# Optimization experiments

Hardware: AMD Instinct MI355X
Metric: run time of the kernel (lower is better)

Reference implementation:

```python
import jax, jax.numpy as jnp
import numpy as np

B, L, E = 2, 2048, 1024
H = 16
DH = E // H  # head dim for qk and v (dim_qk=dim_v=embed_dim)
HID = 4 * E  # fcn_dim_factor * dim_v
SCALE = DH ** 0.5


def setup_inputs() -> dict:
    key = jax.random.key(0)
    ks = jax.random.split(key, 12)
    s = lambda fan_in: 1.0 / np.sqrt(fan_in)
    return {
        "x": jax.random.uniform(ks[0], (B, L), jnp.float32),
        "z": jax.random.normal(ks[1], (B, L, E), jnp.float32),
        "Wq": jax.random.normal(ks[2], (E, E), jnp.float32) * s(E),
        "bq": jnp.zeros((E,), jnp.float32),
        "Wk": jax.random.normal(ks[3], (E, E), jnp.float32) * s(E),
        "bk": jnp.zeros((E,), jnp.float32),
        "Wv": jax.random.normal(ks[4], (E, E), jnp.float32) * s(E),
        "bv": jnp.zeros((E,), jnp.float32),
        "W1": jax.random.normal(ks[5], (E, HID), jnp.float32) * s(E),
        "b1": jnp.zeros((HID,), jnp.float32),
        "W2": jax.random.normal(ks[6], (HID, 1), jnp.float32) * s(HID),
        "b2": jnp.zeros((1,), jnp.float32),
    }


def reference(x, z, Wq, bq, Wk, bk, Wv, bv, W1, b1, W2, b2):
    # Projections -> (B, H, L, DH)
    def heads(t):
        return t.reshape(B, L, H, DH).transpose(0, 2, 1, 3)

    Q = heads(z @ Wq + bq)
    K = heads(z @ Wk + bk)
    V = heads(z @ Wv + bv)

    # Scores (B, H, L, L)
    S = jnp.einsum("bhid,bhjd->bhij", Q, K) / SCALE

    # Weighted softmax along query axis (dim=-2), weighted by population x
    w = x[:, None, :, None]  # (B, 1, L, 1), broadcasts over queries i
    m = jnp.max(S, axis=-2, keepdims=True)
    e = w * jnp.exp(S - m)
    A = e / jnp.sum(e, axis=-2, keepdims=True)

    # V scaled by population weight, then AV
    V_scaled = w * V
    O = jnp.einsum("bhij,bhjd->bhid", A, V_scaled)  # (B, H, L, DH)
    O = O.transpose(0, 2, 1, 3).reshape(B, L, H * DH)

    # FFN: Linear -> GELU (exact) -> Linear(->1) -> squeeze
    y = jax.nn.gelu(O @ W1 + b1, approximate=False)
    y = (y @ W2 + b2).squeeze(-1)  # (B, L)
    return y
```

## Files before the change

kernel.cpp:

```cpp
#include <hip/hip_runtime.h>
#include <hip/hip_bf16.h>
#include <math.h>

#define B_    2
#define L_    2048
#define E_    1024
#define H_    16
#define DH_   64
#define HID_  4096
#define NROW_ (B_*L_)
#define BH_   (B_*H_)

#define QSCL  0.18033688011112042f

typedef __attribute__((ext_vector_type(8)))  short    short8v;
typedef _Float16 half8v __attribute__((ext_vector_type(8)));
typedef __attribute__((ext_vector_type(16))) float    f32x16;

#define MFMA32(A, Bv, C) __builtin_amdgcn_mfma_f32_32x32x16_bf16((A), (Bv), (C), 0, 0, 0)
#define MFMAH(A, Bv, C)  __builtin_amdgcn_mfma_f32_32x32x16_f16((A), (Bv), (C), 0, 0, 0)

__device__ __forceinline__ unsigned short f2bf(float f) {
    union { float f; unsigned u; } v; v.f = f;
    return (unsigned short)((v.u + 0x8000u) >> 16);
}
__device__ __forceinline__ unsigned pack2_bf16(float lo, float hi) {
    union { float f; unsigned u; } a, b; a.f = lo; b.f = hi;
    return __builtin_amdgcn_perm(b.u + 0x8000u, a.u + 0x8000u, 0x07060302u);
}
__device__ __forceinline__ float bf2f(unsigned short u) {
    union { unsigned u; float f; } v; v.u = ((unsigned)u) << 16;
    return v.f;
}

__device__ __forceinline__ void gl_lds16(const void* g, void* l) {
    __builtin_amdgcn_global_load_lds(
        (const __attribute__((address_space(1))) unsigned int*)g,
        (__attribute__((address_space(3))) unsigned int*)l, 16, 0, 0);
}

__device__ __forceinline__ float erf_fast(float v) {
    float a = fabsf(v);
    float t = __builtin_amdgcn_rcpf(1.0f + 0.3275911f * a);
    float p = t * (0.254829592f + t * (-0.284496736f + t * (1.421413741f +
              t * (-1.453152027f + t * 1.061405429f))));
    float r = 1.0f - p * __expf(-a * a);
    return copysignf(r, v);
}

__global__ __launch_bounds__(256) void zh_prep(
    const float* __restrict__ z, _Float16* __restrict__ zh)
{
    const size_t i = ((size_t)blockIdx.x * 256 + threadIdx.x) * 8;
    float4 a = *(const float4*)&z[i];
    float4 b = *(const float4*)&z[i + 4];
    union { _Float16 h[8]; half8v v; } o;
    o.h[0] = (_Float16)a.x; o.h[1] = (_Float16)a.y;
    o.h[2] = (_Float16)a.z; o.h[3] = (_Float16)a.w;
    o.h[4] = (_Float16)b.x; o.h[5] = (_Float16)b.y;
    o.h[6] = (_Float16)b.z; o.h[7] = (_Float16)b.w;
    *(half8v*)&zh[i] = o.v;
}

__global__ __launch_bounds__(256) void wprep3(
    const float* __restrict__ Wq, const float* __restrict__ Wk,
    const float* __restrict__ Wv,
    _Float16* __restrict__ Tq, _Float16* __restrict__ Tk,
    _Float16* __restrict__ Tv)
{
    const float* src = (blockIdx.z == 0) ? Wq : (blockIdx.z == 1) ? Wk : Wv;
    _Float16*    dst = (blockIdx.z == 0) ? Tq : (blockIdx.z == 1) ? Tk : Tv;
    __shared__ float tile[64][65];
    const int t  = threadIdx.x;
    const int r0 = blockIdx.y * 64, c0 = blockIdx.x * 64;
    #pragma unroll
    for (int u = 0; u < 4; ++u) {
        int f = t + 256 * u, row = f >> 4, c4 = (f & 15) << 2;
        *(float4*)&tile[row][c4] = *(const float4*)&src[(size_t)(r0 + row) * E_ + c0 + c4];
    }
    __syncthreads();
    #pragma unroll
    for (int u = 0; u < 4; ++u) {
        int f = t + 256 * u, c = f >> 4, r4 = (f & 15) << 2;
        union { _Float16 h[4]; uint2 u2; } pk;
        pk.h[0] = (_Float16)tile[r4 + 0][c];
        pk.h[1] = (_Float16)tile[r4 + 1][c];
        pk.h[2] = (_Float16)tile[r4 + 2][c];
        pk.h[3] = (_Float16)tile[r4 + 3][c];
        *(uint2*)&dst[(size_t)(c0 + c) * E_ + r0 + r4] = pk.u2;
    }
}

__global__ __launch_bounds__(256) void w1prep(
    const float* __restrict__ W1, _Float16* __restrict__ W1t)
{
    __shared__ float tile[64][65];
    const int t  = threadIdx.x;
    const int r0 = blockIdx.y * 64, c0 = blockIdx.x * 64;
    #pragma unroll
    for (int u = 0; u < 4; ++u) {
        int f = t + 256 * u, row = f >> 4, c4 = (f & 15) << 2;
        *(float4*)&tile[row][c4] = *(const float4*)&W1[(size_t)(r0 + row) * HID_ + c0 + c4];
    }
    __syncthreads();
    #pragma unroll
    for (int u = 0; u < 4; ++u) {
        int f = t + 256 * u, c = f >> 4, r4 = (f & 15) << 2;
        union { _Float16 h[4]; uint2 u2; } pk;
        pk.h[0] = (_Float16)tile[r4 + 0][c];
        pk.h[1] = (_Float16)tile[r4 + 1][c];
        pk.h[2] = (_Float16)tile[r4 + 2][c];
        pk.h[3] = (_Float16)tile[r4 + 3][c];
        *(uint2*)&W1t[(size_t)(c0 + c) * E_ + r0 + r4] = pk.u2;
    }
}

__global__ __launch_bounds__(256) void qkv_mfma(
    const _Float16* __restrict__ zh,
    const _Float16* __restrict__ Tq, const _Float16* __restrict__ Tk,
    const _Float16* __restrict__ Tv,
    const float* __restrict__ bq, const float* __restrict__ bk,
    const float* __restrict__ bv,
    unsigned short* __restrict__ Qo, unsigned short* __restrict__ Ko,
    unsigned short* __restrict__ Vo)
{
    const int which = blockIdx.z;
    const _Float16* Wt = (which == 0) ? Tq : (which == 1) ? Tk : Tv;
    const float*  bias = (which == 0) ? bq : (which == 1) ? bk : bv;
    unsigned short* out = (which == 0) ? Qo : (which == 1) ? Ko : Vo;
    const float   osc  = (which == 0) ? QSCL : 1.0f;

    __shared__ _Float16 Ah[128 * 64];
    __shared__ _Float16 Bs[128 * 64];

    const int t    = threadIdx.x;
    const int lane = t & 63;
    const int w    = t >> 6;
    const int l31  = lane & 31;
    const int hq   = lane >> 5;
    const int wm   = w >> 1, wn = w & 1;
    const int m0   = blockIdx.x * 128;
    const int n0   = blockIdx.y * 128;

    const int srow0 = (lane >> 3);
    const int ssl   = lane & 7;

    f32x16 acc[2][2] = {};

    for (int kc = 0; kc < 16; ++kc) {
        __syncthreads();
        #pragma unroll
        for (int u = 0; u < 4; ++u) {
            int ch  = w * 4 + u;
            int row = ch * 8 + srow0;
            gl_lds16(&zh[(size_t)(m0 + row) * E_ + kc * 64 + ((ssl ^ (row & 7)) << 3)], &Ah[ch * 512]);
            gl_lds16(&Wt[(size_t)(n0 + row) * E_ + kc * 64 + ((ssl ^ (row & 7)) << 3)], &Bs[ch * 512]);
        }
        __syncthreads();

        #pragma unroll
        for (int ks = 0; ks < 4; ++ks) {
            half8v fb[2];
            #pragma unroll
            for (int nb = 0; nb < 2; ++nb) {
                int br = wn * 64 + nb * 32 + l31;
                fb[nb] = *(const half8v*)&Bs[br * 64 + (((ks * 2 + hq) ^ (br & 7)) << 3)];
            }
            #pragma unroll
            for (int mb = 0; mb < 2; ++mb) {
                int ar = wm * 64 + mb * 32 + l31;
                half8v fa = *(const half8v*)&Ah[ar * 64 + (((ks * 2 + hq) ^ (ar & 7)) << 3)];
                acc[mb][0] = MFMAH(fa, fb[0], acc[mb][0]);
                acc[mb][1] = MFMAH(fa, fb[1], acc[mb][1]);
            }
        }
    }

    #pragma unroll
    for (int nb = 0; nb < 2; ++nb) {
        int n  = n0 + wn * 64 + nb * 32 + l31;
        int h  = n >> 6, dh = n & 63;
        float bb = bias[n];
        #pragma unroll
        for (int mb = 0; mb < 2; ++mb) {
            #pragma unroll
            for (int r = 0; r < 16; ++r) {
                int m  = m0 + wm * 64 + mb * 32 + (r & 3) + 8 * (r >> 2) + 4 * hq;
                int b  = m >> 11, i = m & (L_ - 1);
                out[((size_t)(b * H_ + h) * L_ + i) * DH_ + dh] = f2bf((acc[mb][nb][r] + bb) * osc);
            }
        }
    }
}

__global__ __launch_bounds__(256) void col_stats_mfma(
    const unsigned short* __restrict__ Qb, const unsigned short* __restrict__ Kb,
    const float* __restrict__ x, float* __restrict__ Do)
{
    __shared__ unsigned short Qlds[2][128 * 64];
    __shared__ float xlds[L_];

    const int t    = threadIdx.x;
    const int lane = t & 63;
    const int wv   = t >> 6;
    const int l31  = lane & 31;
    const int hq   = lane >> 5;
    const int bh   = blockIdx.y;
    const int b    = bh >> 4;
    const int j0   = blockIdx.x * 128 + wv * 32;

    const int srow0 = (lane >> 3);
    const int ssl   = lane & 7;

    #pragma unroll
    for (int u = 0; u < 2; ++u) {
        int f = t + 256 * u;
        *(float4*)&xlds[f * 4] = *(const float4*)&x[(size_t)b * L_ + f * 4];
    }

    short8v kf[4];
    {
        const unsigned short* kp = Kb + ((size_t)bh * L_ + j0 + l31) * DH_ + hq * 8;
        #pragma unroll
        for (int c = 0; c < 4; ++c) kf[c] = *(const short8v*)(kp + c * 16);
    }

    float d[16];
    #pragma unroll
    for (int r = 0; r < 16; ++r) d[r] = 0.f;

#define CS_STAGE(bb, ich)                                                           \
    {                                                                               \
        _Pragma("unroll")                                                           \
        for (int u = 0; u < 4; ++u) {                                               \
            int ch  = wv * 4 + u;                                                   \
            int row = ch * 8 + srow0;                                               \
            gl_lds16(&Qb[((size_t)bh * L_ + (ich) * 128 + row) * DH_ + ((ssl ^ (row & 7)) << 3)], \
                     &Qlds[bb][ch * 512]);                                          \
        }                                                                           \
    }

    CS_STAGE(0, 0);
    __syncthreads();
    int cur = 0;

    for (int ich = 0; ich < L_ / 128; ++ich) {
        if (ich < L_ / 128 - 1) CS_STAGE(cur ^ 1, ich + 1);

        #pragma unroll
        for (int cc = 0; cc < 4; ++cc) {
            f32x16 acc = {};
            __builtin_amdgcn_s_setprio(1);
            #pragma unroll
            for (int c = 0; c < 4; ++c) {
                int qr = cc * 32 + l31;
                short8v qv = *(const short8v*)&Qlds[cur][qr * 64 + (((c * 2 + hq) ^ (qr & 7)) << 3)];
                acc = MFMA32(kf[c], qv, acc);
            }
            __builtin_amdgcn_s_setprio(0);
            float xi = xlds[ich * 128 + cc * 32 + l31];
            #pragma unroll
            for (int r = 0; r < 16; ++r)
                d[r] += xi * __builtin_amdgcn_exp2f(acc[r]);
        }
        __syncthreads();
        cur ^= 1;
    }

    #pragma unroll
    for (int r = 0; r < 16; ++r) {
        #pragma unroll
        for (int off = 16; off > 0; off >>= 1)
            d[r] += __shfl_xor(d[r], off);
    }
    if (l31 == 0) {
        #pragma unroll
        for (int r = 0; r < 16; ++r)
            Do[(size_t)bh * L_ + j0 + 4 * hq + (r & 3) + 8 * (r >> 2)] = d[r];
    }
#undef CS_STAGE
}

__global__ __launch_bounds__(256) void vt_prep(
    const unsigned short* __restrict__ Vb, const float* __restrict__ x,
    const float* __restrict__ Do, unsigned short* __restrict__ Vt)
{
    const int bh = blockIdx.y;
    const int b  = bh >> 4;
    const int j  = blockIdx.x * 256 + threadIdx.x;
    const float s = x[(size_t)b * L_ + j] / Do[(size_t)bh * L_ + j];
    const unsigned short* vp = Vb + ((size_t)bh * L_ + j) * DH_;
    #pragma unroll
    for (int c = 0; c < 16; ++c) {
        ushort4 v = *(const ushort4*)&vp[c * 4];
        Vt[((size_t)bh * DH_ + c * 4 + 0) * L_ + j] = f2bf(bf2f(v.x) * s);
        Vt[((size_t)bh * DH_ + c * 4 + 1) * L_ + j] = f2bf(bf2f(v.y) * s);
        Vt[((size_t)bh * DH_ + c * 4 + 2) * L_ + j] = f2bf(bf2f(v.z) * s);
        Vt[((size_t)bh * DH_ + c * 4 + 3) * L_ + j] = f2bf(bf2f(v.w) * s);
    }
}

__global__ __launch_bounds__(256) void attn_out_mfma(
    const unsigned short* __restrict__ Qb, const unsigned short* __restrict__ Kb,
    const unsigned short* __restrict__ Vt, const float* __restrict__ x,
    _Float16* __restrict__ Of)
{
    __shared__ unsigned short Klds[2][64 * 64];
    __shared__ unsigned short Vlds[2][64 * 64];

    const int t    = threadIdx.x;
    const int lane = t & 63;
    const int wv   = t >> 6;
    const int l31  = lane & 31;
    const int hq   = lane >> 5;
    const int bh   = blockIdx.y;
    const int b    = bh >> 4, hh = bh & 15;
    const int iw   = blockIdx.x * 128 + wv * 32;

    const int srow0 = (lane >> 3);
    const int ssl   = lane & 7;

    short8v qf[4];
    {
        const unsigned short* qp = Qb + ((size_t)bh * L_ + iw + l31) * DH_ + hq * 8;
        #pragma unroll
        for (int c = 0; c < 4; ++c) qf[c] = *(const short8v*)(qp + c * 16);
    }

    f32x16 accO0 = {}, accO1 = {};

#define AO_STAGE(bb, jt)                                                            \
    {                                                                               \
        _Pragma("unroll")                                                           \
        for (int u = 0; u < 2; ++u) {                                               \
            int ch  = wv * 2 + u;                                                   \
            int row = ch * 8 + srow0;                                               \
            gl_lds16(&Kb[((size_t)bh * L_ + (jt) * 64 + row) * DH_ + ((ssl ^ (row & 7)) << 3)], \
                     &Klds[bb][ch * 512]);                                          \
            gl_lds16(&Vt[((size_t)bh * DH_ + row) * L_ + (jt) * 64 + ((ssl ^ (row & 7)) << 3)], \
                     &Vlds[bb][ch * 512]);                                          \
        }                                                                           \
    }

    AO_STAGE(0, 0);
    __syncthreads();
    int cur = 0;

    for (int jt = 0; jt < L_ / 64; ++jt) {
        if (jt < L_ / 64 - 1) AO_STAGE(cur ^ 1, jt + 1);

        uint4 pa[4];
        #pragma unroll
        for (int js = 0; js < 2; ++js) {
            f32x16 as = {};
            __builtin_amdgcn_s_setprio(1);
            #pragma unroll
            for (int c = 0; c < 4; ++c) {
                int krow = js * 32 + l31;
                short8v kfr = *(const short8v*)&Klds[cur][krow * 64 + (((c * 2 + hq) ^ (krow & 7)) << 3)];
                as = MFMA32(kfr, qf[c], as);
            }
            __builtin_amdgcn_s_setprio(0);
            float p[16];
            #pragma unroll
            for (int r = 0; r < 16; ++r) p[r] = __builtin_amdgcn_exp2f(as[r]);

            unsigned P0 = pack2_bf16(p[0], p[1]);
            unsigned P1 = pack2_bf16(p[2], p[3]);
            unsigned Q0 = pack2_bf16(p[4], p[5]);
            unsigned Q1 = pack2_bf16(p[6], p[7]);
            asm("v_permlane32_swap_b32 %0, %1" : "+v"(P0), "+v"(Q0));
            asm("v_permlane32_swap_b32 %0, %1" : "+v"(P1), "+v"(Q1));
            pa[js * 2 + 0] = make_uint4(P0, P1, Q0, Q1);

            unsigned R0 = pack2_bf16(p[8],  p[9]);
            unsigned R1 = pack2_bf16(p[10], p[11]);
            unsigned S0 = pack2_bf16(p[12], p[13]);
            unsigned S1 = pack2_bf16(p[14], p[15]);
            asm("v_permlane32_swap_b32 %0, %1" : "+v"(R0), "+v"(S0));
            asm("v_permlane32_swap_b32 %0, %1" : "+v"(R1), "+v"(S1));
            pa[js * 2 + 1] = make_uint4(R0, R1, S0, S1);
        }

        __builtin_amdgcn_s_setprio(1);
        #pragma unroll
        for (int c = 0; c < 4; ++c) {
            union { uint4 u; short8v s; } paf; paf.u = pa[c];
            int r0 = l31, r1 = 32 + l31;
            short8v vf0 = *(const short8v*)&Vlds[cur][r0 * 64 + (((c * 2 + hq) ^ (r0 & 7)) << 3)];
            short8v vf1 = *(const short8v*)&Vlds[cur][r1 * 64 + (((c * 2 + hq) ^ (r1 & 7)) << 3)];
            accO0 = MFMA32(paf.s, vf0, accO0);
            accO1 = MFMA32(paf.s, vf1, accO1);
        }
        __builtin_amdgcn_s_setprio(0);
        __syncthreads();
        cur ^= 1;
    }

    #pragma unroll
    for (int q = 0; q < 4; ++q) {
        float4 xq = *(const float4*)&x[(size_t)b * L_ + iw + 4 * hq + 8 * q];
        const float xs[4] = { xq.x, xq.y, xq.z, xq.w };
        #pragma unroll
        for (int k = 0; k < 4; ++k) {
            int r    = q * 4 + k;
            int irow = iw + 4 * hq + 8 * q + k;
            size_t base = ((size_t)b * L_ + irow) * E_ + hh * DH_;
            Of[base + l31]      = (_Float16)(accO0[r] * xs[k]);
            Of[base + 32 + l31] = (_Float16)(accO1[r] * xs[k]);
        }
    }
#undef AO_STAGE
}

__global__ __launch_bounds__(256) void y_init(float* __restrict__ y, const float* __restrict__ b2)
{
    y[blockIdx.x * 256 + threadIdx.x] = b2[0];
}

__global__ __launch_bounds__(256) void mlp_mfma(
    const _Float16* __restrict__ Of, const _Float16* __restrict__ W1t,
    const float* __restrict__ b1, const float* __restrict__ W2,
    float* __restrict__ y)
{
    __shared__ _Float16 Oh[128 * 64];
    __shared__ _Float16 Wh[128 * 64];

    const int t    = threadIdx.x;
    const int lane = t & 63;
    const int w    = t >> 6;
    const int l31  = lane & 31;
    const int hq   = lane >> 5;
    const int wm   = w >> 1, wn = w & 1;
    const int m0   = blockIdx.x * 128;
    const int n0   = blockIdx.y * 128;

    const int srow0 = (lane >> 3);
    const int ssl   = lane & 7;

    f32x16 acc[2][2] = {};

    for (int kc = 0; kc < 16; ++kc) {
        __syncthreads();
        #pragma unroll
        for (int u = 0; u < 4; ++u) {
            int ch  = w * 4 + u;
            int row = ch * 8 + srow0;
            gl_lds16(&Of[(size_t)(m0 + row) * E_ + kc * 64 + ((ssl ^ (row & 7)) << 3)], &Oh[ch * 512]);
            gl_lds16(&W1t[(size_t)(n0 + row) * E_ + kc * 64 + ((ssl ^ (row & 7)) << 3)], &Wh[ch * 512]);
        }
        __syncthreads();

        #pragma unroll
        for (int ks = 0; ks < 4; ++ks) {
            half8v fb[2];
            #pragma unroll
            for (int nb = 0; nb < 2; ++nb) {
                int br = wn * 64 + nb * 32 + l31;
                fb[nb] = *(const half8v*)&Wh[br * 64 + (((ks * 2 + hq) ^ (br & 7)) << 3)];
            }
            #pragma unroll
            for (int mb = 0; mb < 2; ++mb) {
                int ar = wm * 64 + mb * 32 + l31;
                half8v fa = *(const half8v*)&Oh[ar * 64 + (((ks * 2 + hq) ^ (ar & 7)) << 3)];
                acc[mb][0] = MFMAH(fa, fb[0], acc[mb][0]);
                acc[mb][1] = MFMAH(fa, fb[1], acc[mb][1]);
            }
        }
    }

    const int hid0 = n0 + wn * 64 + l31;
    const float bb0 = b1[hid0],      w20 = W2[hid0];
    const float bb1 = b1[hid0 + 32], w21 = W2[hid0 + 32];
    #pragma unroll
    for (int mb = 0; mb < 2; ++mb) {
        #pragma unroll
        for (int r = 0; r < 16; ++r) {
            float h0 = acc[mb][0][r] + bb0;
            float h1 = acc[mb][1][r] + bb1;
            float s  = 0.5f * h0 * (1.0f + erf_fast(h0 * 0.70710678f)) * w20
                     + 0.5f * h1 * (1.0f + erf_fast(h1 * 0.70710678f)) * w21;
            #pragma unroll
            for (int off = 16; off > 0; off >>= 1) s += __shfl_xor(s, off);
            if (l31 == 0) {
                int m = m0 + wm * 64 + mb * 32 + (r & 3) + 8 * (r >> 2) + 4 * hq;
                atomicAdd(&y[m], s);
            }
        }
    }
}

extern "C" void kernel_launch(void* const* d_in, const int* in_sizes, int n_in,
                              void* d_out, int out_size, void* d_ws, size_t ws_size,
                              hipStream_t stream)
{
    const float* x  = (const float*)d_in[0];
    const float* z  = (const float*)d_in[1];
    const float* Wq = (const float*)d_in[2];
    const float* bq = (const float*)d_in[3];
    const float* Wk = (const float*)d_in[4];
    const float* bk = (const float*)d_in[5];
    const float* Wv = (const float*)d_in[6];
    const float* bv = (const float*)d_in[7];
    const float* W1 = (const float*)d_in[8];
    const float* b1 = (const float*)d_in[9];
    const float* W2 = (const float*)d_in[10];
    const float* b2 = (const float*)d_in[11];
    float* y = (float*)d_out;

    const size_t NQ = (size_t)BH_ * L_ * DH_;
    unsigned short* p = (unsigned short*)d_ws;
    unsigned short* Qb  = p;  p += NQ;
    unsigned short* Kb  = p;  p += NQ;
    unsigned short* Vb  = p;  p += NQ;
    unsigned short* Vt  = p;  p += NQ;
    _Float16* zh  = (_Float16*)p;  p += (size_t)NROW_ * E_;
    _Float16* Tq  = (_Float16*)p;  p += (size_t)E_ * E_;
    _Float16* Tk  = (_Float16*)p;  p += (size_t)E_ * E_;
    _Float16* Tv  = (_Float16*)p;  p += (size_t)E_ * E_;
    _Float16* W1t = (_Float16*)p;  p += (size_t)HID_ * E_;
    _Float16* Ofp = (_Float16*)p;  p += (size_t)NROW_ * E_;
    float* Dw = (float*)p;

    zh_prep<<<dim3((NROW_ * E_) / (256 * 8)), 256, 0, stream>>>(z, zh);
    wprep3 <<<dim3(E_ / 64, E_ / 64, 3), 256, 0, stream>>>(Wq, Wk, Wv, Tq, Tk, Tv);
    w1prep <<<dim3(HID_ / 64, E_ / 64), 256, 0, stream>>>(W1, W1t);

    qkv_mfma<<<dim3(NROW_ / 128, E_ / 128, 3), 256, 0, stream>>>(
        zh, Tq, Tk, Tv, bq, bk, bv, Qb, Kb, Vb);

    col_stats_mfma<<<dim3(L_ / 128, BH_), 256, 0, stream>>>(Qb, Kb, x, Dw);

    vt_prep<<<dim3(L_ / 256, BH_), 256, 0, stream>>>(Vb, x, Dw, Vt);

    attn_out_mfma<<<dim3(L_ / 128, BH_), 256, 0, stream>>>(Qb, Kb, Vt, x, Ofp);

    y_init<<<dim3(NROW_ / 256), 256, 0, stream>>>(y, b2);

    mlp_mfma<<<dim3(NROW_ / 128, HID_ / 128), 256, 0, stream>>>(
        Ofp, W1t, b1, W2, y);
}
```

Baseline: 217.4 us.

## Double-buffer LDS staging with vmcnt-based waits across all four MFMA kernels

Converts the QKV and MLP GEMM kernels from single-buffered load-then-compute loops to two-stage LDS double buffering. All four MFMA kernels now prefetch two tiles ahead and use explicit s_waitcnt vmcnt plus raw s_barrier in place of __syncthreads. The goal is to overlap global-to-LDS async loads with MFMA work and avoid full drains each iteration. In exchange LDS per block doubles in the GEMMs, which may reduce occupancy, and correctness now depends on the hand-counted vmcnt values.

Result: faster. 207.5 us (-4.6%).

```diff
diff --git a/kernel.cpp b/kernel.cpp
--- a/kernel.cpp
+++ b/kernel.cpp
@@ -19,6 +19,9 @@
 
 #define MFMA32(A, Bv, C) __builtin_amdgcn_mfma_f32_32x32x16_bf16((A), (Bv), (C), 0, 0, 0)
 #define MFMAH(A, Bv, C)  __builtin_amdgcn_mfma_f32_32x32x16_f16((A), (Bv), (C), 0, 0, 0)
+
+#define WAITV(N) asm volatile("s_waitcnt vmcnt(" #N ")" ::: "memory")
+#define SBAR()   __builtin_amdgcn_s_barrier()
 
 __device__ __forceinline__ unsigned short f2bf(float f) {
     union { float f; unsigned u; } v; v.f = f;
@@ -130,8 +133,8 @@
     unsigned short* out = (which == 0) ? Qo : (which == 1) ? Ko : Vo;
     const float   osc  = (which == 0) ? QSCL : 1.0f;
 
-    __shared__ _Float16 Ah[128 * 64];
-    __shared__ _Float16 Bs[128 * 64];
+    __shared__ _Float16 Ah[2][128 * 64];
+    __shared__ _Float16 Bs[2][128 * 64];
 
     const int t    = threadIdx.x;
     const int lane = t & 63;
@@ -147,33 +150,48 @@
 
     f32x16 acc[2][2] = {};
 
+#define QKV_STAGE(bb, kc)                                                          \
+    {                                                                              \
+        _Pragma("unroll")                                                          \
+        for (int u = 0; u < 4; ++u) {                                              \
+            int ch  = w * 4 + u;                                                   \
+            int row = ch * 8 + srow0;                                              \
+            gl_lds16(&zh[(size_t)(m0 + row) * E_ + (kc) * 64 + ((ssl ^ (row & 7)) << 3)], \
+                     &Ah[bb][ch * 512]);                                           \
+            gl_lds16(&Wt[(size_t)(n0 + row) * E_ + (kc) * 64 + ((ssl ^ (row & 7)) << 3)], \
+                     &Bs[bb][ch * 512]);                                           \
+        }                                                                          \
+    }
+
+    QKV_STAGE(0, 0);
+    QKV_STAGE(1, 1);
+    __syncthreads();
+    int cur = 0;
+
     for (int kc = 0; kc < 16; ++kc) {
-        __syncthreads();
-        #pragma unroll
-        for (int u = 0; u < 4; ++u) {
-            int ch  = w * 4 + u;
-            int row = ch * 8 + srow0;
-            gl_lds16(&zh[(size_t)(m0 + row) * E_ + kc * 64 + ((ssl ^ (row & 7)) << 3)], &Ah[ch * 512]);
-            gl_lds16(&Wt[(size_t)(n0 + row) * E_ + kc * 64 + ((ssl ^ (row & 7)) << 3)], &Bs[ch * 512]);
-        }
-        __syncthreads();
-
+        if (kc < 15) WAITV(8); else WAITV(0);
+        SBAR();
+        __builtin_amdgcn_s_setprio(1);
         #pragma unroll
         for (int ks = 0; ks < 4; ++ks) {
             half8v fb[2];
             #pragma unroll
             for (int nb = 0; nb < 2; ++nb) {
                 int br = wn * 64 + nb * 32 + l31;
-                fb[nb] = *(const half8v*)&Bs[br * 64 + (((ks * 2 + hq) ^ (br & 7)) << 3)];
+                fb[nb] = *(const half8v*)&Bs[cur][br * 64 + (((ks * 2 + hq) ^ (br & 7)) << 3)];
             }
             #pragma unroll
             for (int mb = 0; mb < 2; ++mb) {
                 int ar = wm * 64 + mb * 32 + l31;
-                half8v fa = *(const half8v*)&Ah[ar * 64 + (((ks * 2 + hq) ^ (ar & 7)) << 3)];
+                half8v fa = *(const half8v*)&Ah[cur][ar * 64 + (((ks * 2 + hq) ^ (ar & 7)) << 3)];
                 acc[mb][0] = MFMAH(fa, fb[0], acc[mb][0]);
                 acc[mb][1] = MFMAH(fa, fb[1], acc[mb][1]);
             }
         }
+        __builtin_amdgcn_s_setprio(0);
+        SBAR();
+        if (kc + 2 < 16) QKV_STAGE(cur, kc + 2);
+        cur ^= 1;
     }
 
     #pragma unroll
@@ -191,6 +209,7 @@
             }
         }
     }
+#undef QKV_STAGE
 }
 
 __global__ __launch_bounds__(256) void col_stats_mfma(
@@ -241,12 +260,14 @@
     }
 
     CS_STAGE(0, 0);
+    CS_STAGE(1, 1);
     __syncthreads();
     int cur = 0;
 
-    for (int ich = 0; ich < L_ / 128; ++ich) {
-        if (ich < L_ / 128 - 1) CS_STAGE(cur ^ 1, ich + 1);
-
+    const int NT = L_ / 128;
+    for (int ich = 0; ich < NT; ++ich) {
+        if (ich < NT - 1) WAITV(4); else WAITV(0);
+        SBAR();
         #pragma unroll
         for (int cc = 0; cc < 4; ++cc) {
             f32x16 acc = {};
@@ -263,7 +284,8 @@
             for (int r = 0; r < 16; ++r)
                 d[r] += xi * __builtin_amdgcn_exp2f(acc[r]);
         }
-        __syncthreads();
+        SBAR();
+        if (ich + 2 < NT) CS_STAGE(cur, ich + 2);
         cur ^= 1;
     }
 
@@ -343,11 +365,14 @@
     }
 
     AO_STAGE(0, 0);
+    AO_STAGE(1, 1);
     __syncthreads();
     int cur = 0;
 
-    for (int jt = 0; jt < L_ / 64; ++jt) {
-        if (jt < L_ / 64 - 1) AO_STAGE(cur ^ 1, jt + 1);
+    const int NT = L_ / 64;
+    for (int jt = 0; jt < NT; ++jt) {
+        if (jt < NT - 1) WAITV(4); else WAITV(0);
+        SBAR();
 
         uint4 pa[4];
         #pragma unroll
@@ -393,7 +418,8 @@
             accO1 = MFMA32(paf.s, vf1, accO1);
         }
         __builtin_amdgcn_s_setprio(0);
-        __syncthreads();
+        SBAR();
+        if (jt + 2 < NT) AO_STAGE(cur, jt + 2);
         cur ^= 1;
     }
 
@@ -423,8 +449,8 @@
     const float* __restrict__ b1, const float* __restrict__ W2,
     float* __restrict__ y)
 {
-    __shared__ _Float16 Oh[128 * 64];
-    __shared__ _Float16 Wh[128 * 64];
+    __shared__ _Float16 Oh[2][128 * 64];
+    __shared__ _Float16 Wh[2][128 * 64];
 
     const int t    = threadIdx.x;
     const int lane = t & 63;
@@ -440,33 +466,48 @@
 
     f32x16 acc[2][2] = {};
 
+#define MLP_STAGE(bb, kc)                                                          \
+    {                                                                              \
+        _Pragma("unroll")                                                          \
+        for (int u = 0; u < 4; ++u) {                                              \
+            int ch  = w * 4 + u;                                                   \
+            int row = ch * 8 + srow0;                                              \
+            gl_lds16(&Of[(size_t)(m0 + row) * E_ + (kc) * 64 + ((ssl ^ (row & 7)) << 3)], \
+                     &Oh[bb][ch * 512]);                                           \
+            gl_lds16(&W1t[(size_t)(n0 + row) * E_ + (kc) * 64 + ((ssl ^ (row & 7)) << 3)], \
+                     &Wh[bb][ch * 512]);                                           \
+        }                                                                          \
+    }
+
+    MLP_STAGE(0, 0);
+    MLP_STAGE(1, 1);
+    __syncthreads();
+    int cur = 0;
+
     for (int kc = 0; kc < 16; ++kc) {
-        __syncthreads();
-        #pragma unroll
-        for (int u = 0; u < 4; ++u) {
-            int ch  = w * 4 + u;
-            int row = ch * 8 + srow0;
-            gl_lds16(&Of[(size_t)(m0 + row) * E_ + kc * 64 + ((ssl ^ (row & 7)) << 3)], &Oh[ch * 512]);
-            gl_lds16(&W1t[(size_t)(n0 + row) * E_ + kc * 64 + ((ssl ^ (row & 7)) << 3)], &Wh[ch * 512]);
-        }
-        __syncthreads();
-
+        if (kc < 15) WAITV(8); else WAITV(0);
+        SBAR();
+        __builtin_amdgcn_s_setprio(1);
         #pragma unroll
         for (int ks = 0; ks < 4; ++ks) {
             half8v fb[2];
             #pragma unroll
             for (int nb = 0; nb < 2; ++nb) {
                 int br = wn * 64 + nb * 32 + l31;
-                fb[nb] = *(const half8v*)&Wh[br * 64 + (((ks * 2 + hq) ^ (br & 7)) << 3)];
+                fb[nb] = *(const half8v*)&Wh[cur][br * 64 + (((ks * 2 + hq) ^ (br & 7)) << 3)];
             }
             #pragma unroll
             for (int mb = 0; mb < 2; ++mb) {
                 int ar = wm * 64 + mb * 32 + l31;
-                half8v fa = *(const half8v*)&Oh[ar * 64 + (((ks * 2 + hq) ^ (ar & 7)) << 3)];
+                half8v fa = *(const half8v*)&Oh[cur][ar * 64 + (((ks * 2 + hq) ^ (ar & 7)) << 3)];
                 acc[mb][0] = MFMAH(fa, fb[0], acc[mb][0]);
                 acc[mb][1] = MFMAH(fa, fb[1], acc[mb][1]);
             }
         }
+        __builtin_amdgcn_s_setprio(0);
+        SBAR();
+        if (kc + 2 < 16) MLP_STAGE(cur, kc + 2);
+        cur ^= 1;
     }
 
     const int hid0 = n0 + wn * 64 + l31;
@@ -488,6 +529,7 @@
             }
         }
     }
+#undef MLP_STAGE
 }
 
 extern "C" void kernel_launch(void* const* d_in, const int* in_sizes, int n_in,
```
